# Optimization experiments

Hardware: AMD Instinct MI355X
Metric: run time of the kernel (lower is better)

Reference implementation:

```python
import jax, jax.numpy as jnp
import numpy as np

D = 1024
H = 16
DH = D // H
MAX_TYPES = 256
B, L = 8, 1024
EPS = 1e-5


def setup_inputs() -> dict:
    key = jax.random.key(0)
    ks = jax.random.split(key, 16)
    s = 0.02
    return {
        'type_ids': jax.random.randint(ks[0], (B, L), 0, MAX_TYPES),
        'values': jax.random.normal(ks[1], (B, L, 1), jnp.float32),
        'deltas': jax.random.uniform(ks[2], (B, L, 1), jnp.float32),
        'type_emb': jax.random.normal(ks[3], (MAX_TYPES, D), jnp.float32) * s,
        'Wv': jax.random.normal(ks[4], (D, 1), jnp.float32) * s,
        'bv': jnp.zeros((D,), jnp.float32),
        'Wt': jax.random.normal(ks[5], (D, 1), jnp.float32) * s,
        'bt': jnp.zeros((D,), jnp.float32),
        'Win': jax.random.normal(ks[6], (3 * D, D), jnp.float32) * s,
        'bin': jnp.zeros((3 * D,), jnp.float32),
        'Wout': jax.random.normal(ks[7], (D, D), jnp.float32) * s,
        'bout': jnp.zeros((D,), jnp.float32),
        'W1': jax.random.normal(ks[8], (D, D), jnp.float32) * s,
        'b1': jnp.zeros((D,), jnp.float32),
        'W2': jax.random.normal(ks[9], (D, D), jnp.float32) * s,
        'b2': jnp.zeros((D,), jnp.float32),
        'gamma': jnp.ones((D,), jnp.float32),
        'beta': jnp.zeros((D,), jnp.float32),
    }


def _ln(x, gamma, beta):
    mu = jnp.mean(x, axis=-1, keepdims=True)
    var = jnp.mean(jnp.square(x - mu), axis=-1, keepdims=True)
    return (x - mu) * jax.lax.rsqrt(var + EPS) * gamma + beta


def reference(type_ids, values, deltas, type_emb, Wv, bv, Wt, bt,
              Win, bin, Wout, bout, W1, b1, W2, b2, gamma, beta):
    # fused embedding: type lookup + value/time linear projections
    h = type_emb[type_ids] + values @ Wv.T + bv + deltas @ Wt.T + bt  # [B,L,D]
    b, l, d = h.shape
    # multi-head self-attention (explicit weights path, need_weights=True)
    qkv = h @ Win.T + bin  # [B,L,3D]
    q, k, v = jnp.split(qkv, 3, axis=-1)
    q = q.reshape(b, l, H, DH)
    k = k.reshape(b, l, H, DH)
    v = v.reshape(b, l, H, DH)
    scale = 1.0 / jnp.sqrt(jnp.asarray(DH, h.dtype))
    scores = jnp.einsum('blhd,bmhd->bhlm', q, k) * scale  # [B,H,L,L]
    w = jax.nn.softmax(scores, axis=-1)
    attn = jnp.einsum('bhlm,bmhd->blhd', w, v).reshape(b, l, d)
    attn_out = attn @ Wout.T + bout
    h2 = _ln(h + attn_out, gamma, beta)
    ff = jax.nn.relu(h2 @ W1.T + b1) @ W2.T + b2
    h3 = _ln(h2 + ff, gamma, beta)
    pooled = h3.mean(axis=1)  # [B,D]
    attn_tokens = w.mean(axis=1).mean(axis=2)  # mean over heads, then keys -> [B,L]
    return pooled, attn_tokens
```

## Files before the change

### kernel.cpp

```cpp
#include <hip/hip_runtime.h>
#include <hip/hip_bf16.h>


#define Dm 1024
#define Hh 16
#define Bb 8
#define Ll 1024
#define Mm 8192
#define LNEPS 1e-5f
#define QSCALE 0.18033688f

typedef __attribute__((ext_vector_type(8))) short s16x8;
typedef __attribute__((ext_vector_type(4))) short s16x4;
typedef __attribute__((ext_vector_type(4))) float f32x4;
typedef __attribute__((ext_vector_type(16))) float f32x16;

using bf16 = __hip_bfloat16;

__device__ __forceinline__ short f2bs(float f) {
  return __builtin_bit_cast(short, __float2bfloat16(f));
}
__device__ __forceinline__ float b2f(short s) {
  return __builtin_bit_cast(float, ((unsigned)(unsigned short)s) << 16);
}

__device__ __forceinline__ unsigned cvtpk(float lo, float hi) {
  unsigned r;
  asm("v_cvt_pk_bf16_f32 %0, %1, %2" : "=v"(r) : "v"(lo), "v"(hi));
  return r;
}
__device__ __forceinline__ void perm32(unsigned &a, unsigned &b) {
  asm volatile("v_permlane32_swap_b32 %0, %1" : "+v"(a), "+v"(b));
}

__device__ __forceinline__ void gload16(const void* g, void* l) {
  __builtin_amdgcn_global_load_lds(
      (__attribute__((address_space(1))) void*)g,
      (__attribute__((address_space(3))) void*)l, 16, 0, 0);
}

__global__ __launch_bounds__(256) void k_f2b4(
    const float* __restrict__ w0, const float* __restrict__ w1,
    const float* __restrict__ w2, const float* __restrict__ w3,
    bf16* __restrict__ o0, bf16* __restrict__ o1,
    bf16* __restrict__ o2, bf16* __restrict__ o3)
{
  const int bId = blockIdx.x;
  const float* src; bf16* dst; int rel;
  float sc = 1.f;
  if (bId < 3072)      { src = w0; dst = o0; rel = bId; if (bId < 1024) sc = QSCALE; }
  else if (bId < 4096) { src = w1; dst = o1; rel = bId - 3072; }
  else if (bId < 5120) { src = w2; dst = o2; rel = bId - 4096; }
  else                 { src = w3; dst = o3; rel = bId - 5120; }
  const size_t i = ((size_t)rel * 256 + threadIdx.x) * 4;
  const float4 v = *(const float4*)&src[i];
  s16x4 o;
  o[0] = f2bs(v.x * sc); o[1] = f2bs(v.y * sc); o[2] = f2bs(v.z * sc); o[3] = f2bs(v.w * sc);
  *(s16x4*)&dst[i] = o;
}

__global__ __launch_bounds__(256) void k_embed(
    const int* __restrict__ tids, const float* __restrict__ vals, const float* __restrict__ dels,
    const float* __restrict__ temb, const float* __restrict__ Wv, const float* __restrict__ bv,
    const float* __restrict__ Wt, const float* __restrict__ bt,
    bf16* __restrict__ hb)
{
  const int row = blockIdx.x;
  const int ty = tids[row];
  const float v = vals[row], dl = dels[row];
  const int d0 = threadIdx.x * 4;
  const float4 e  = *(const float4*)&temb[(size_t)ty * Dm + d0];
  const float4 wv = *(const float4*)&Wv[d0];
  const float4 c1 = *(const float4*)&bv[d0];
  const float4 wt = *(const float4*)&Wt[d0];
  const float4 c2 = *(const float4*)&bt[d0];
  s16x4 o;
  o[0] = f2bs(e.x + v * wv.x + c1.x + dl * wt.x + c2.x);
  o[1] = f2bs(e.y + v * wv.y + c1.y + dl * wt.y + c2.y);
  o[2] = f2bs(e.z + v * wv.z + c1.z + dl * wt.z + c2.z);
  o[3] = f2bs(e.w + v * wv.w + c1.w + dl * wt.w + c2.w);
  *(s16x4*)((short*)hb + (size_t)row * Dm + d0) = o;
}

template<bool RELU, bool RES, bool QS>
__global__ __launch_bounds__(512) void k_gemm8(
    const bf16* __restrict__ A, const bf16* __restrict__ Bt,
    const float* __restrict__ bias, const bf16* __restrict__ res,
    bf16* __restrict__ outB, const int N, const int K)
{
  __shared__ __attribute__((aligned(16))) short lds[49152];
  const int tid = threadIdx.x, lane = tid & 63, wave = tid >> 6;
  const int wr = wave >> 2, wc = wave & 3;
  const int l15 = lane & 15, lg = (lane >> 4) & 3;
  const int bm = blockIdx.x, bn = blockIdx.y;
  const int NT = K >> 6;

  const int rl = tid >> 3;
  const int swz = ((tid & 7) ^ (rl & 7)) * 8;
  const bf16* aSrc = A  + (size_t)(bm * 128 + rl) * K + swz;
  const bf16* bSrc = Bt + (size_t)(bn * 256 + rl) * K + swz;

  f32x4 acc[4][4] = {};

  auto stageA = [&](int t, int h) {
    gload16(aSrc + (size_t)h * 64 * K + t * 64,
            &lds[(t & 1) * 24576 + h * 4096 + tid * 8]);
  };
  auto stageB = [&](int t, int h) {
    gload16(bSrc + (size_t)h * 128 * K + t * 64,
            &lds[(t & 1) * 24576 + 8192 + h * 8192 + tid * 8]);
    gload16(bSrc + (size_t)(h * 128 + 64) * K + t * 64,
            &lds[(t & 1) * 24576 + 8192 + h * 8192 + 4096 + tid * 8]);
  };

  stageA(0, 0); stageA(0, 1); stageB(0, 0); stageB(0, 1);
  if (NT > 1) { stageA(1, 0); stageA(1, 1); }
  asm volatile("s_waitcnt vmcnt(2)" ::: "memory");
  __builtin_amdgcn_sched_barrier(0);
  __builtin_amdgcn_s_barrier();

  for (int t = 0; t < NT; ++t) {
    const int cb = (t & 1) * 24576;
    s16x8 fa[4][2], fb[2][2];

#pragma unroll
    for (int m = 0; m < 4; ++m)
#pragma unroll
      for (int ks = 0; ks < 2; ++ks) {
        const int row = wr * 64 + m * 16 + l15;
        fa[m][ks] = *(const s16x8*)&lds[cb + row * 64 + (((ks * 4 + lg) ^ (row & 7)) << 3)];
      }
#pragma unroll
    for (int n = 0; n < 2; ++n)
#pragma unroll
      for (int ks = 0; ks < 2; ++ks) {
        const int row = wc * 64 + n * 16 + l15;
        fb[n][ks] = *(const s16x8*)&lds[cb + 8192 + row * 64 + (((ks * 4 + lg) ^ (row & 7)) << 3)];
      }
    if (t + 1 < NT) { stageB(t + 1, 0); stageB(t + 1, 1); }
    __builtin_amdgcn_s_barrier();
    asm volatile("s_waitcnt lgkmcnt(0)" ::: "memory");
    __builtin_amdgcn_sched_barrier(0);
    __builtin_amdgcn_s_setprio(1);
#pragma unroll
    for (int m = 0; m < 4; ++m)
#pragma unroll
      for (int n = 0; n < 2; ++n)
#pragma unroll
        for (int ks = 0; ks < 2; ++ks)
          acc[m][n] = __builtin_amdgcn_mfma_f32_16x16x32_bf16(fa[m][ks], fb[n][ks], acc[m][n], 0, 0, 0);
    __builtin_amdgcn_s_setprio(0);
    __builtin_amdgcn_s_barrier();

#pragma unroll
    for (int n = 0; n < 2; ++n)
#pragma unroll
      for (int ks = 0; ks < 2; ++ks) {
        const int row = wc * 64 + (2 + n) * 16 + l15;
        fb[n][ks] = *(const s16x8*)&lds[cb + 8192 + row * 64 + (((ks * 4 + lg) ^ (row & 7)) << 3)];
      }
    if (t + 2 < NT) { stageA(t + 2, 0); stageA(t + 2, 1); }
    __builtin_amdgcn_s_barrier();
    asm volatile("s_waitcnt lgkmcnt(0)" ::: "memory");
    __builtin_amdgcn_sched_barrier(0);
    __builtin_amdgcn_s_setprio(1);
#pragma unroll
    for (int m = 0; m < 4; ++m)
#pragma unroll
      for (int n = 0; n < 2; ++n)
#pragma unroll
        for (int ks = 0; ks < 2; ++ks)
          acc[m][2 + n] = __builtin_amdgcn_mfma_f32_16x16x32_bf16(fa[m][ks], fb[n][ks], acc[m][2 + n], 0, 0, 0);
    __builtin_amdgcn_s_setprio(0);

    if (t + 1 < NT) {
      if (t + 2 < NT) asm volatile("s_waitcnt vmcnt(2)" ::: "memory");
      else            asm volatile("s_waitcnt vmcnt(0)" ::: "memory");
      __builtin_amdgcn_sched_barrier(0);
      __builtin_amdgcn_s_barrier();
    }
  }

#pragma unroll
  for (int n = 0; n < 4; ++n) {
    const int col = bn * 256 + wc * 64 + n * 16 + l15;
    float bc = bias[col];
    if constexpr (QS) { if (col < 1024) bc *= QSCALE; }
#pragma unroll
    for (int m = 0; m < 4; ++m) {
#pragma unroll
      for (int i = 0; i < 4; ++i) {
        const size_t row = (size_t)bm * 128 + wr * 64 + m * 16 + lg * 4 + i;
        float v = acc[m][n][i] + bc;
        if constexpr (RES)  v += b2f(((const short*)res)[row * N + col]);
        if constexpr (RELU) v = fmaxf(v, 0.f);
        outB[row * N + col] = __float2bfloat16(v);
      }
    }
  }
}

__global__ __launch_bounds__(256) void k_vt(const bf16* __restrict__ qkv, bf16* __restrict__ vt)
{
  const int bh = blockIdx.x, lc = blockIdx.y;
  const int b = bh >> 4, h = bh & 15;
  __shared__ short tile[64][72];
  const int r = threadIdx.x >> 2;
  const int c0 = (threadIdx.x & 3) << 4;
  const short* src = (const short*)qkv + ((size_t)(b * Ll + lc * 64 + r)) * 3072 + 2048 + h * 64 + c0;
  const s16x8 x0 = *(const s16x8*)src;
  const s16x8 x1 = *(const s16x8*)(src + 8);
#pragma unroll
  for (int j = 0; j < 8; ++j) { tile[r][c0 + j] = x0[j]; tile[r][c0 + 8 + j] = x1[j]; }
  __syncthreads();
  s16x8 y0, y1;
#pragma unroll
  for (int j = 0; j < 8; ++j) { y0[j] = tile[c0 + j][r]; y1[j] = tile[c0 + 8 + j][r]; }
  short* dst = (short*)vt + ((size_t)(bh * 64 + r)) * Ll + lc * 64 + c0;
  *(s16x8*)dst = y0;
  *(s16x8*)(dst + 8) = y1;
}

__global__ __launch_bounds__(256) void k_attn(
    const bf16* __restrict__ qkv, const bf16* __restrict__ vt, bf16* __restrict__ attnb)
{
  const int bh = blockIdx.x, qb = blockIdx.y;
  const int b = bh >> 4, h = bh & 15;
  __shared__ __attribute__((aligned(16))) short lK[8192];
  __shared__ __attribute__((aligned(16))) short lV[8192];
  const int tid = threadIdx.x, lane = tid & 63, wave = tid >> 6;
  const int l31 = lane & 31, hi = lane >> 5;
  const int r7 = l31 & 7;
  const int qbase = qb * 256 + wave * 64;

  s16x8 qf[2][4];
#pragma unroll
  for (int g = 0; g < 2; ++g) {
    const short* qp = (const short*)qkv +
        ((size_t)(b * Ll + qbase + g * 32 + l31)) * 3072 + h * 64 + hi * 8;
#pragma unroll
    for (int s = 0; s < 4; ++s) qf[g][s] = *(const s16x8*)(qp + s * 16);
  }

  f32x16 o[2][2] = {};
  float rsa[2][4] = {};

  const int sr = tid >> 3;
  const int swz = (tid & 7) ^ (sr & 7);

  auto stage = [&](int mc) {
    const int bo = (mc & 1) * 4096;
    const bf16* gk = qkv + ((size_t)(b * Ll + mc * 64 + sr)) * 3072 + 1024 + h * 64 + swz * 8;
    gload16(gk,                      &lK[bo + tid * 8]);
    gload16(gk + (size_t)32 * 3072,  &lK[bo + 2048 + tid * 8]);
    const bf16* gv = vt + ((size_t)(bh * 64 + sr)) * Ll + mc * 64 + swz * 8;
    gload16(gv,                    &lV[bo + tid * 8]);
    gload16(gv + (size_t)32 * Ll,  &lV[bo + 2048 + tid * 8]);
  };

  stage(0);

  for (int mc = 0; mc < 16; ++mc) {
    asm volatile("s_waitcnt vmcnt(0)" ::: "memory");
    __builtin_amdgcn_s_barrier();
    __builtin_amdgcn_sched_barrier(0);
    if (mc + 1 < 16) stage(mc + 1);
    const int bo = (mc & 1) * 4096;

    s16x8 kf[4][2], vf[4][2];
#pragma unroll
    for (int s = 0; s < 4; ++s) {
      const int sl = (((2 * s + hi) ^ r7) << 3);
      kf[s][0] = *(const s16x8*)&lK[bo + l31 * 64 + sl];
      kf[s][1] = *(const s16x8*)&lK[bo + (32 + l31) * 64 + sl];
      vf[s][0] = *(const s16x8*)&lV[bo + l31 * 64 + sl];
      vf[s][1] = *(const s16x8*)&lV[bo + (32 + l31) * 64 + sl];
    }

#pragma unroll
    for (int g = 0; g < 2; ++g) {
      f32x16 st0 = {}, st1 = {};
      __builtin_amdgcn_s_setprio(1);
#pragma unroll
      for (int s = 0; s < 4; ++s) {
        st0 = __builtin_amdgcn_mfma_f32_32x32x16_bf16(kf[s][0], qf[g][s], st0, 0, 0, 0);
        st1 = __builtin_amdgcn_mfma_f32_32x32x16_bf16(kf[s][1], qf[g][s], st1, 0, 0, 0);
      }
      __builtin_amdgcn_s_setprio(0);

#pragma unroll
      for (int r = 0; r < 16; ++r) {
        const float e0 = __builtin_amdgcn_exp2f(st0[r]);
        const float e1 = __builtin_amdgcn_exp2f(st1[r]);
        rsa[g][r & 3] += e0 + e1;
        st0[r] = e0; st1[r] = e1;
      }

      __builtin_amdgcn_s_setprio(1);
#pragma unroll
      for (int ss = 0; ss < 4; ++ss) {
        const f32x16& src = (ss < 2) ? st0 : st1;
        const int go = (ss & 1) * 8;
        unsigned c0 = cvtpk(src[go + 0], src[go + 1]);
        unsigned c1 = cvtpk(src[go + 2], src[go + 3]);
        unsigned c2 = cvtpk(src[go + 4], src[go + 5]);
        unsigned c3 = cvtpk(src[go + 6], src[go + 7]);
        perm32(c0, c2);
        perm32(c1, c3);
        uint4 wda; wda.x = c0; wda.y = c1; wda.z = c2; wda.w = c3;
        const s16x8 pa = __builtin_bit_cast(s16x8, wda);
        o[g][0] = __builtin_amdgcn_mfma_f32_32x32x16_bf16(pa, vf[ss][0], o[g][0], 0, 0, 0);
        o[g][1] = __builtin_amdgcn_mfma_f32_32x32x16_bf16(pa, vf[ss][1], o[g][1], 0, 0, 0);
      }
      __builtin_amdgcn_s_setprio(0);
    }
  }

#pragma unroll
  for (int g = 0; g < 2; ++g) {
    float rs = (rsa[g][0] + rsa[g][1]) + (rsa[g][2] + rsa[g][3]);
    rs += __shfl_xor(rs, 32);
    float inv[16];
#pragma unroll
    for (int r = 0; r < 16; ++r)
      inv[r] = 1.f / __shfl(rs, (r & 3) + 8 * (r >> 2) + 4 * hi);
#pragma unroll
    for (int t = 0; t < 2; ++t) {
#pragma unroll
      for (int r = 0; r < 16; ++r) {
        const int q = qbase + g * 32 + (r & 3) + 8 * (r >> 2) + 4 * hi;
        attnb[((size_t)(b * Ll + q)) * Dm + h * 64 + t * 32 + l31] =
            __float2bfloat16(o[g][t][r] * inv[r]);
      }
    }
  }
}

__global__ __launch_bounds__(256) void k_ln(const bf16* __restrict__ x,
    const float* __restrict__ gamma, const float* __restrict__ beta,
    bf16* __restrict__ y)
{
  const size_t row = blockIdx.x;
  const int d0 = threadIdx.x * 4;
  const s16x4 xv = *(const s16x4*)((const short*)x + row * Dm + d0);
  float f0 = b2f(xv[0]), f1 = b2f(xv[1]), f2 = b2f(xv[2]), f3 = b2f(xv[3]);
  float s  = (f0 + f1) + (f2 + f3);
  float ss = (f0 * f0 + f1 * f1) + (f2 * f2 + f3 * f3);
#pragma unroll
  for (int m = 1; m < 64; m <<= 1) { s += __shfl_xor(s, m); ss += __shfl_xor(ss, m); }
  __shared__ float red[8];
  const int wv = threadIdx.x >> 6;
  if ((threadIdx.x & 63) == 0) { red[wv] = s; red[4 + wv] = ss; }
  __syncthreads();
  s  = red[0] + red[1] + red[2] + red[3];
  ss = red[4] + red[5] + red[6] + red[7];
  const float mu = s * (1.f / Dm);
  const float rstd = rsqrtf(ss * (1.f / Dm) - mu * mu + LNEPS);
  const float4 g  = *(const float4*)&gamma[d0];
  const float4 be = *(const float4*)&beta[d0];
  s16x4 o;
  o[0] = f2bs((f0 - mu) * rstd * g.x + be.x);
  o[1] = f2bs((f1 - mu) * rstd * g.y + be.y);
  o[2] = f2bs((f2 - mu) * rstd * g.z + be.z);
  o[3] = f2bs((f3 - mu) * rstd * g.w + be.w);
  *(s16x4*)((short*)y + row * Dm + d0) = o;
}

__global__ __launch_bounds__(256) void k_pool_part(const bf16* __restrict__ h3, float* __restrict__ part)
{
  const int b = blockIdx.x, lcn = blockIdx.y, dz = blockIdx.z;
  const int d = dz * 256 + threadIdx.x;
  float s = 0.f;
#pragma unroll 4
  for (int l = 0; l < 64; ++l)
    s += b2f(((const short*)h3)[((size_t)(b * Ll + lcn * 64 + l)) * Dm + d]);
  part[((size_t)(b * 16 + lcn)) * Dm + d] = s;
}

__global__ __launch_bounds__(256) void k_pool_fin(const float* __restrict__ part, float* __restrict__ out)
{
  const int b = blockIdx.x;
  const int d = blockIdx.y * 256 + threadIdx.x;
  float s = 0.f;
#pragma unroll
  for (int c = 0; c < 16; ++c) s += part[((size_t)(b * 16 + c)) * Dm + d];
  out[b * Dm + d] = s * (1.f / Ll);
  out[(size_t)Mm + b * Dm + d] = 1.f / Ll;
}

extern "C" void kernel_launch(void* const* d_in, const int* in_sizes, int n_in,
                              void* d_out, int out_size, void* d_ws, size_t ws_size,
                              hipStream_t stream) {
  const int*   tids  = (const int*)  d_in[0];
  const float* vals  = (const float*)d_in[1];
  const float* dels  = (const float*)d_in[2];
  const float* temb  = (const float*)d_in[3];
  const float* Wv    = (const float*)d_in[4];
  const float* bv    = (const float*)d_in[5];
  const float* Wt    = (const float*)d_in[6];
  const float* bt    = (const float*)d_in[7];
  const float* Win   = (const float*)d_in[8];
  const float* bin   = (const float*)d_in[9];
  const float* Wout  = (const float*)d_in[10];
  const float* bout  = (const float*)d_in[11];
  const float* W1    = (const float*)d_in[12];
  const float* b1    = (const float*)d_in[13];
  const float* W2    = (const float*)d_in[14];
  const float* b2    = (const float*)d_in[15];
  const float* gamma = (const float*)d_in[16];
  const float* beta  = (const float*)d_in[17];
  float* out = (float*)d_out;

  char* w = (char*)d_ws;
  const size_t MB = 1ull << 20;
  bf16*  hb    = (bf16*) (w + 0);
  bf16*  qkv   = (bf16*) (w + 16 * MB);
  bf16*  vtb   = (bf16*) (w + 64 * MB);
  bf16*  attnb = (bf16*) (w + 80 * MB);
  bf16*  x1b   = (bf16*) (w + 16 * MB);
  bf16*  h2b   = (bf16*) (w + 32 * MB);
  bf16*  ff1   = (bf16*) (w + 48 * MB);
  bf16*  x2b   = (bf16*) (w + 64 * MB);
  bf16*  h3b   = (bf16*) (w + 80 * MB);
  bf16*  WinB  = (bf16*) (w + 96 * MB);
  bf16*  WoutB = (bf16*) (w + 102 * MB);
  bf16*  W1B   = (bf16*) (w + 104 * MB);
  bf16*  W2B   = (bf16*) (w + 106 * MB);
  float* part  = (float*)(w + 108 * MB);

  k_f2b4<<<6144, 256, 0, stream>>>(Win, Wout, W1, W2, WinB, WoutB, W1B, W2B);

  k_embed<<<Mm, 256, 0, stream>>>(tids, vals, dels, temb, Wv, bv, Wt, bt, hb);

  k_gemm8<false, false, true><<<dim3(64, 12), 512, 0, stream>>>(
      hb, WinB, bin, nullptr, qkv, 3072, 1024);

  k_vt<<<dim3(128, 16), 256, 0, stream>>>(qkv, vtb);
  k_attn<<<dim3(128, 4), 256, 0, stream>>>(qkv, vtb, attnb);

  k_gemm8<false, true, false><<<dim3(64, 4), 512, 0, stream>>>(
      attnb, WoutB, bout, hb, x1b, 1024, 1024);

  k_ln<<<Mm, 256, 0, stream>>>(x1b, gamma, beta, h2b);

  k_gemm8<true, false, false><<<dim3(64, 4), 512, 0, stream>>>(
      h2b, W1B, b1, nullptr, ff1, 1024, 1024);

  k_gemm8<false, true, false><<<dim3(64, 4), 512, 0, stream>>>(
      ff1, W2B, b2, h2b, x2b, 1024, 1024);

  k_ln<<<Mm, 256, 0, stream>>>(x2b, gamma, beta, h3b);

  k_pool_part<<<dim3(8, 16, 4), 256, 0, stream>>>(h3b, part);
  k_pool_fin<<<dim3(8, 4), 256, 0, stream>>>(part, out);
}
```

Baseline: 247.1 us.

## Load K/V fragments directly from global memory in attention, halve queries per wave

The attention kernel stops staging K and V tiles through double-buffered LDS with barriers. Each wave now loads its K and V MFMA fragments straight from global memory, relying on L1/L2 for reuse. Each wave also handles 32 queries instead of 64, so the grid doubles to 1024 blocks, which cuts register pressure and adds parallelism. The cost is that K/V reuse across waves and query groups now depends on the caches, so global/L2 traffic per FLOP rises, and there is no explicit prefetch to hide load latency.

```diff
diff --git a/kernel.cpp b/kernel.cpp
--- a/kernel.cpp
+++ b/kernel.cpp
@@ -226,112 +226,88 @@
 {
   const int bh = blockIdx.x, qb = blockIdx.y;
   const int b = bh >> 4, h = bh & 15;
-  __shared__ __attribute__((aligned(16))) short lK[8192];
-  __shared__ __attribute__((aligned(16))) short lV[8192];
-  const int tid = threadIdx.x, lane = tid & 63, wave = tid >> 6;
+  const int lane = threadIdx.x & 63, wave = threadIdx.x >> 6;
   const int l31 = lane & 31, hi = lane >> 5;
-  const int r7 = l31 & 7;
-  const int qbase = qb * 256 + wave * 64;
-
-  s16x8 qf[2][4];
-#pragma unroll
-  for (int g = 0; g < 2; ++g) {
+  const int qbase = qb * 128 + wave * 32;
+
+  s16x8 qf[4];
+  {
     const short* qp = (const short*)qkv +
-        ((size_t)(b * Ll + qbase + g * 32 + l31)) * 3072 + h * 64 + hi * 8;
-#pragma unroll
-    for (int s = 0; s < 4; ++s) qf[g][s] = *(const s16x8*)(qp + s * 16);
+        ((size_t)(b * Ll + qbase + l31)) * 3072 + h * 64 + hi * 8;
+#pragma unroll
+    for (int s = 0; s < 4; ++s) qf[s] = *(const s16x8*)(qp + s * 16);
   }
 
-  f32x16 o[2][2] = {};
-  float rsa[2][4] = {};
-
-  const int sr = tid >> 3;
-  const int swz = (tid & 7) ^ (sr & 7);
-
-  auto stage = [&](int mc) {
-    const int bo = (mc & 1) * 4096;
-    const bf16* gk = qkv + ((size_t)(b * Ll + mc * 64 + sr)) * 3072 + 1024 + h * 64 + swz * 8;
-    gload16(gk,                      &lK[bo + tid * 8]);
-    gload16(gk + (size_t)32 * 3072,  &lK[bo + 2048 + tid * 8]);
-    const bf16* gv = vt + ((size_t)(bh * 64 + sr)) * Ll + mc * 64 + swz * 8;
-    gload16(gv,                    &lV[bo + tid * 8]);
-    gload16(gv + (size_t)32 * Ll,  &lV[bo + 2048 + tid * 8]);
-  };
-
-  stage(0);
+  const short* kp0 = (const short*)qkv + ((size_t)(b * Ll + l31)) * 3072 + 1024 + h * 64 + hi * 8;
+  const short* kp1 = kp0 + (size_t)32 * 3072;
+  const short* vp0 = (const short*)vt + ((size_t)(bh * 64 + l31)) * Ll + hi * 8;
+  const short* vp1 = vp0 + (size_t)32 * Ll;
+
+  f32x16 o[2] = {};
+  float rsa[4] = {};
 
   for (int mc = 0; mc < 16; ++mc) {
-    asm volatile("s_waitcnt vmcnt(0)" ::: "memory");
-    __builtin_amdgcn_s_barrier();
-    __builtin_amdgcn_sched_barrier(0);
-    if (mc + 1 < 16) stage(mc + 1);
-    const int bo = (mc & 1) * 4096;
-
-    s16x8 kf[4][2], vf[4][2];
+    const size_t ko = (size_t)(mc * 64) * 3072;
+    const int    vo = mc * 64;
+
+    s16x8 kf0[4], kf1[4], vf0[4], vf1[4];
 #pragma unroll
     for (int s = 0; s < 4; ++s) {
-      const int sl = (((2 * s + hi) ^ r7) << 3);
-      kf[s][0] = *(const s16x8*)&lK[bo + l31 * 64 + sl];
-      kf[s][1] = *(const s16x8*)&lK[bo + (32 + l31) * 64 + sl];
-      vf[s][0] = *(const s16x8*)&lV[bo + l31 * 64 + sl];
-      vf[s][1] = *(const s16x8*)&lV[bo + (32 + l31) * 64 + sl];
-    }
-
-#pragma unroll
-    for (int g = 0; g < 2; ++g) {
-      f32x16 st0 = {}, st1 = {};
-      __builtin_amdgcn_s_setprio(1);
-#pragma unroll
-      for (int s = 0; s < 4; ++s) {
-        st0 = __builtin_amdgcn_mfma_f32_32x32x16_bf16(kf[s][0], qf[g][s], st0, 0, 0, 0);
-        st1 = __builtin_amdgcn_mfma_f32_32x32x16_bf16(kf[s][1], qf[g][s], st1, 0, 0, 0);
-      }
-      __builtin_amdgcn_s_setprio(0);
-
-#pragma unroll
-      for (int r = 0; r < 16; ++r) {
-        const float e0 = __builtin_amdgcn_exp2f(st0[r]);
-        const float e1 = __builtin_amdgcn_exp2f(st1[r]);
-        rsa[g][r & 3] += e0 + e1;
-        st0[r] = e0; st1[r] = e1;
-      }
-
-      __builtin_amdgcn_s_setprio(1);
-#pragma unroll
-      for (int ss = 0; ss < 4; ++ss) {
-        const f32x16& src = (ss < 2) ? st0 : st1;
-        const int go = (ss & 1) * 8;
-        unsigned c0 = cvtpk(src[go + 0], src[go + 1]);
-        unsigned c1 = cvtpk(src[go + 2], src[go + 3]);
-        unsigned c2 = cvtpk(src[go + 4], src[go + 5]);
-        unsigned c3 = cvtpk(src[go + 6], src[go + 7]);
-        perm32(c0, c2);
-        perm32(c1, c3);
-        uint4 wda; wda.x = c0; wda.y = c1; wda.z = c2; wda.w = c3;
-        const s16x8 pa = __builtin_bit_cast(s16x8, wda);
-        o[g][0] = __builtin_amdgcn_mfma_f32_32x32x16_bf16(pa, vf[ss][0], o[g][0], 0, 0, 0);
-        o[g][1] = __builtin_amdgcn_mfma_f32_32x32x16_bf16(pa, vf[ss][1], o[g][1], 0, 0, 0);
-      }
-      __builtin_amdgcn_s_setprio(0);
-    }
+      kf0[s] = *(const s16x8*)(kp0 + ko + s * 16);
+      kf1[s] = *(const s16x8*)(kp1 + ko + s * 16);
+      vf0[s] = *(const s16x8*)(vp0 + vo + s * 16);
+      vf1[s] = *(const s16x8*)(vp1 + vo + s * 16);
+    }
+
+    f32x16 st0 = {}, st1 = {};
+    __builtin_amdgcn_s_setprio(1);
+#pragma unroll
+    for (int s = 0; s < 4; ++s) {
+      st0 = __builtin_amdgcn_mfma_f32_32x32x16_bf16(kf0[s], qf[s], st0, 0, 0, 0);
+      st1 = __builtin_amdgcn_mfma_f32_32x32x16_bf16(kf1[s], qf[s], st1, 0, 0, 0);
+    }
+    __builtin_amdgcn_s_setprio(0);
+
+#pragma unroll
+    for (int r = 0; r < 16; ++r) {
+      const float e0 = __builtin_amdgcn_exp2f(st0[r]);
+      const float e1 = __builtin_amdgcn_exp2f(st1[r]);
+      rsa[r & 3] += e0 + e1;
+      st0[r] = e0; st1[r] = e1;
+    }
+
+    __builtin_amdgcn_s_setprio(1);
+#pragma unroll
+    for (int ss = 0; ss < 4; ++ss) {
+      const f32x16& src = (ss < 2) ? st0 : st1;
+      const int go = (ss & 1) * 8;
+      unsigned c0 = cvtpk(src[go + 0], src[go + 1]);
+      unsigned c1 = cvtpk(src[go + 2], src[go + 3]);
+      unsigned c2 = cvtpk(src[go + 4], src[go + 5]);
+      unsigned c3 = cvtpk(src[go + 6], src[go + 7]);
+      perm32(c0, c2);
+      perm32(c1, c3);
+      uint4 wda; wda.x = c0; wda.y = c1; wda.z = c2; wda.w = c3;
+      const s16x8 pa = __builtin_bit_cast(s16x8, wda);
+      o[0] = __builtin_amdgcn_mfma_f32_32x32x16_bf16(pa, vf0[ss], o[0], 0, 0, 0);
+      o[1] = __builtin_amdgcn_mfma_f32_32x32x16_bf16(pa, vf1[ss], o[1], 0, 0, 0);
+    }
+    __builtin_amdgcn_s_setprio(0);
   }
 
-#pragma unroll
-  for (int g = 0; g < 2; ++g) {
-    float rs = (rsa[g][0] + rsa[g][1]) + (rsa[g][2] + rsa[g][3]);
-    rs += __shfl_xor(rs, 32);
-    float inv[16];
-#pragma unroll
-    for (int r = 0; r < 16; ++r)
-      inv[r] = 1.f / __shfl(rs, (r & 3) + 8 * (r >> 2) + 4 * hi);
-#pragma unroll
-    for (int t = 0; t < 2; ++t) {
-#pragma unroll
-      for (int r = 0; r < 16; ++r) {
-        const int q = qbase + g * 32 + (r & 3) + 8 * (r >> 2) + 4 * hi;
-        attnb[((size_t)(b * Ll + q)) * Dm + h * 64 + t * 32 + l31] =
-            __float2bfloat16(o[g][t][r] * inv[r]);
-      }
+  float rs = (rsa[0] + rsa[1]) + (rsa[2] + rsa[3]);
+  rs += __shfl_xor(rs, 32);
+  float inv[16];
+#pragma unroll
+  for (int r = 0; r < 16; ++r)
+    inv[r] = 1.f / __shfl(rs, (r & 3) + 8 * (r >> 2) + 4 * hi);
+#pragma unroll
+  for (int t = 0; t < 2; ++t) {
+#pragma unroll
+    for (int r = 0; r < 16; ++r) {
+      const int q = qbase + (r & 3) + 8 * (r >> 2) + 4 * hi;
+      attnb[((size_t)(b * Ll + q)) * Dm + h * 64 + t * 32 + l31] =
+          __float2bfloat16(o[t][r] * inv[r]);
     }
   }
 }
@@ -436,7 +412,7 @@
       hb, WinB, bin, nullptr, qkv, 3072, 1024);
 
   k_vt<<<dim3(128, 16), 256, 0, stream>>>(qkv, vtb);
-  k_attn<<<dim3(128, 4), 256, 0, stream>>>(qkv, vtb, attnb);
+  k_attn<<<dim3(128, 8), 256, 0, stream>>>(qkv, vtb, attnb);
 
   k_gemm8<false, true, false><<<dim3(64, 4), 512, 0, stream>>>(
       attnb, WoutB, bout, hb, x1b, 1024, 1024);
```

New measurement: 299.1 us. +21.1%, slower.
